# Kernel tuning notes

Hardware: AMD Instinct MI355X
Metric: run time of the kernel (lower is better)

## Reference

```python
import jax, jax.numpy as jnp
import numpy as np
from functools import partial

DN = ('NCHW', 'OIHW', 'NCHW')

def conv2d(x, w, b, stride):
    y = jax.lax.conv_general_dilated(x, w, (stride, stride), 'VALID', dimension_numbers=DN)
    return y + b[None, :, None, None]

def squash(s, eps=1e-8):
    norm = jnp.linalg.norm(s, axis=-1, keepdims=True)
    return (norm ** 2 / (1 + norm ** 2)) * s / (norm + eps)

def setup_inputs() -> dict:
    key = jax.random.key(0)
    ks = jax.random.split(key, 10)
    B, H, W = 16, 32, 512
    F, CAPS, E, OD = 64, 8, 8, 16
    H1 = (H - 6) // 2 + 1          # 14
    W1 = (W - 6) // 2 + 1          # 254
    N = F * H1 * W1 // CAPS        # 28448
    s = 0.05
    return {
        'x': jax.random.normal(ks[0], (B, H, W), jnp.float32),
        'conv1_w': jax.random.normal(ks[1], (F, 1, 6, 6), jnp.float32) * s,
        'conv1_b': jnp.zeros((F,), jnp.float32),
        'conv2_w': jax.random.normal(ks[2], (F, F, 6, 6), jnp.float32) * s,
        'conv2_b': jnp.zeros((F,), jnp.float32),
        'conv3_w': jax.random.normal(ks[3], (F, 2 * F, 1, 1), jnp.float32) * s,
        'conv3_b': jnp.zeros((F,), jnp.float32),
        'pc_w': jax.random.normal(ks[4], (N, CAPS, CAPS), jnp.float32) * s,  # [N, in, out]
        'pc_b': jnp.zeros((N, CAPS), jnp.float32),
        'ec_w': jax.random.normal(ks[5], (N, E, OD, CAPS), jnp.float32),
    }

def reference(x, conv1_w, conv1_b, conv2_w, conv2_b, conv3_w, conv3_b, pc_w, pc_b, ec_w):
    CAPS = pc_w.shape[1]
    NUM_ITER = 3
    B = x.shape[0]
    h = x[:, None]                                  # [B,1,H,W]
    h = jax.nn.relu(conv2d(h, conv1_w, conv1_b, 2)) # [B,F,14,254]
    y = jnp.pad(h, ((0, 0), (0, 0), (2, 3), (2, 3)))  # ZeroPad2d((2,3,2,3))
    y = jax.nn.relu(conv2d(y, conv2_w, conv2_b, 1))
    h = jax.nn.relu(jnp.concatenate((h, y), axis=1))
    h = conv2d(h, conv3_w, conv3_b, 1)              # [B,F,14,254]
    u_in = h.reshape(B, -1, CAPS)                   # [B,N,caps_len]
    # PrimaryCaps: N independent Linear(caps,caps) -> one batched einsum
    u = jnp.einsum('bni,nio->bno', u_in, pc_w) + pc_b[None]
    # EmotionCaps: per-capsule prediction u_hat [B,N,E,out_dim]
    u_hat = jnp.einsum('neoi,bni->bneo', ec_w, u)
    N, E = ec_w.shape[0], ec_w.shape[1]
    b_log = jnp.zeros((B, N, E), u_hat.dtype)
    v = None
    for r in range(NUM_ITER):
        c = jax.nn.softmax(b_log, axis=2)           # [B,N,E]
        s = jnp.einsum('bne,bneo->beo', c, u_hat)   # [B,E,out_dim]
        v = squash(s)
        if r < NUM_ITER - 1:
            b_log = b_log + jnp.einsum('bneo,beo->bne', u_hat, v)
    return jnp.linalg.norm(v, axis=-1)              # [B,E]
```

## Files before the change

### kernel.cpp

```cpp
#include <hip/hip_runtime.h>
#include <hip/hip_bf16.h>
#include <math.h>

#define BB 16
#define H1 14
#define W1 254
#define HPH 19
#define HPW2 264
#define NCAP 28448
#define FLATSZ 227584

typedef __attribute__((ext_vector_type(8))) short bf16x8;
typedef __attribute__((ext_vector_type(4))) float f32x4;
typedef __attribute__((ext_vector_type(2))) __fp16 f16x2;
typedef __attribute__((ext_vector_type(8))) _Float16 h8;
typedef __attribute__((ext_vector_type(4))) uint uint4v;

__device__ __forceinline__ ushort f2bf(float f) {
  __hip_bfloat16 h = __float2bfloat16(f);
  return *(ushort*)&h;
}

__global__ __launch_bounds__(256) void prep_w(const float* __restrict__ w2, const float* __restrict__ w3,
                                              ushort* __restrict__ wb, float* __restrict__ w3t) {
  int idx = blockIdx.x * 256 + threadIdx.x;
  if (idx < 147456) {
    int co = idx / 2304; int rem = idx - co * 2304;
    int tap = rem >> 6; int ci = rem & 63;
    wb[idx] = f2bf(w2[(co * 64 + ci) * 36 + tap]);
  }
  if (idx < 8192) {
    int co = idx & 63; int c = idx >> 6;
    w3t[idx] = w3[co * 128 + c];
  }
}

__global__ __launch_bounds__(256) void cvt_ec(const float* __restrict__ ecw, uint* __restrict__ ech) {
  size_t i = (size_t)blockIdx.x * 256 + threadIdx.x;
  const float4* s = (const float4*)ecw + i * 2;
  float4 a = s[0], b = s[1];
  uint4v pk;
  { f16x2 h = __builtin_amdgcn_cvt_pkrtz(a.x, a.y); pk.x = *(uint*)&h; }
  { f16x2 h = __builtin_amdgcn_cvt_pkrtz(a.z, a.w); pk.y = *(uint*)&h; }
  { f16x2 h = __builtin_amdgcn_cvt_pkrtz(b.x, b.y); pk.z = *(uint*)&h; }
  { f16x2 h = __builtin_amdgcn_cvt_pkrtz(b.z, b.w); pk.w = *(uint*)&h; }
  *((uint4v*)ech + i) = pk;
}

__global__ __launch_bounds__(256) void cvt_u(const float* __restrict__ u, _Float16* __restrict__ uh) {
  const int idx = blockIdx.x * 256 + threadIdx.x;
  const int n = idx >> 4, b = idx & 15;
  const float4* s = (const float4*)(u + ((size_t)b * NCAP + n) * 8);
  float4 xa = s[0], xb = s[1];
  h8 o;
  o[0] = (_Float16)xa.x; o[1] = (_Float16)xa.y; o[2] = (_Float16)xa.z; o[3] = (_Float16)xa.w;
  o[4] = (_Float16)xb.x; o[5] = (_Float16)xb.y; o[6] = (_Float16)xb.z; o[7] = (_Float16)xb.w;
  *(h8*)(uh + (size_t)idx * 8) = o;
}

__global__ __launch_bounds__(256) void conv1_k(const float* __restrict__ x, const float* __restrict__ w1,
                                               const float* __restrict__ b1, float* __restrict__ hc) {
  const int i = blockIdx.x, b = blockIdx.y;
  __shared__ float xs[6 * 512];
  __shared__ float wsh[2304];
  __shared__ float bsh[64];
  const int t = threadIdx.x;
  for (int idx = t; idx < 6 * 512; idx += 256) {
    int r = idx >> 9, c = idx & 511;
    xs[idx] = x[((size_t)b * 32 + 2 * i + r) * 512 + c];
  }
  for (int idx = t; idx < 2304; idx += 256) wsh[idx] = w1[idx];
  if (t < 64) bsh[t] = b1[t];
  __syncthreads();
  if (t < 254) {
    for (int c = 0; c < 64; c++) {
      float acc = bsh[c];
#pragma unroll
      for (int p = 0; p < 6; p++)
#pragma unroll
        for (int q = 0; q < 6; q++)
          acc = fmaf(xs[p * 512 + 2 * t + q], wsh[c * 36 + p * 6 + q], acc);
      acc = fmaxf(acc, 0.f);
      hc[(((size_t)b * 64 + c) * H1 + i) * W1 + t] = acc;
    }
  }
}

__global__ __launch_bounds__(256) void nhwc_k(const float* __restrict__ hc, ushort* __restrict__ hpc) {
  const int ct = blockIdx.x, i = blockIdx.y, b = blockIdx.z;
  const int c0 = ct * 64;
  __shared__ float ls[64 * 65];
  const int t = threadIdx.x;
  for (int idx = t; idx < 4096; idx += 256) {
    int ci = idx >> 6, cc = idx & 63;
    int c = c0 + cc;
    ls[ci * 65 + cc] = (c < W1) ? hc[(((size_t)b * 64 + ci) * H1 + i) * W1 + c] : 0.f;
  }
  __syncthreads();
  uint* outp = (uint*)hpc;
  for (int idx = t; idx < 2048; idx += 256) {
    int cc = idx >> 5, ci2 = idx & 31;
    int c = c0 + cc;
    if (c < W1) {
      float f0 = ls[(2 * ci2) * 65 + cc];
      float f1 = ls[(2 * ci2 + 1) * 65 + cc];
      uint pk = (uint)f2bf(f0) | ((uint)f2bf(f1) << 16);
      outp[(((size_t)b * HPH + 2 + i) * HPW2 + 2 + c) * 32 + ci2] = pk;
    }
  }
}

__device__ __forceinline__ void stage_b(const ushort* __restrict__ wb, ushort* __restrict__ bbuf,
                                        int tap, int w, int l) {
#pragma unroll
  for (int r = 0; r < 2; r++) {
    int v = r * 256 + w * 64 + l;
    int co = v >> 3, s = v & 7;
    int g = s ^ (co & 7);
    const ushort* gp = wb + co * 2304 + tap * 64 + g * 8;
    ushort* lp = bbuf + (size_t)(r * 256 + w * 64) * 8;
    __builtin_amdgcn_global_load_lds((const uint*)gp, (uint*)lp, 16, 0, 0);
  }
}

__global__ __launch_bounds__(256, 1) void conv2_mfma(const ushort* __restrict__ hpc,
                                                     const ushort* __restrict__ wb,
                                                     const float* __restrict__ b2, float* __restrict__ y) {
  const int b = blockIdx.z, i = blockIdx.y, j0 = blockIdx.x * 128;
  const int t = threadIdx.x;
  const int w = t >> 6, l = t & 63;
  const int lr = l & 15, quad = l >> 4;

  __shared__ ushort bls[2][4096];

  f32x4 acc[2][4];
#pragma unroll
  for (int mt = 0; mt < 2; mt++)
#pragma unroll
    for (int nt = 0; nt < 4; nt++) acc[mt][nt] = (f32x4){0.f, 0.f, 0.f, 0.f};

  const ushort* abase = hpc + (((size_t)b * HPH + i) * HPW2 + (j0 + w * 32 + lr)) * 64 + quad * 8;

  bf16x8 a0[2][2], a1[2][2];

#define ALOAD(dst, tap)                                                        \
  {                                                                            \
    const int p_ = (tap) / 6, q_ = (tap) % 6;                                  \
    const ushort* ap_ = abase + ((size_t)p_ * HPW2 + q_) * 64;                 \
    dst[0][0] = *(const bf16x8*)(ap_);                                         \
    dst[0][1] = *(const bf16x8*)(ap_ + 1024);                                  \
    dst[1][0] = *(const bf16x8*)(ap_ + 32);                                    \
    dst[1][1] = *(const bf16x8*)(ap_ + 32 + 1024);                             \
  }

#define COMPUTE(a, bp)                                                         \
  {                                                                            \
    _Pragma("unroll")                                                          \
    for (int ch = 0; ch < 2; ch++) {                                           \
      const int g2 = ch * 4 + quad;                                            \
      _Pragma("unroll")                                                        \
      for (int nt = 0; nt < 4; nt++) {                                         \
        const int co = nt * 16 + lr;                                           \
        bf16x8 bf = *(const bf16x8*)((bp) + co * 64 + ((g2 ^ (co & 7)) * 8));  \
        acc[0][nt] = __builtin_amdgcn_mfma_f32_16x16x32_bf16(a[ch][0], bf, acc[0][nt], 0, 0, 0); \
        acc[1][nt] = __builtin_amdgcn_mfma_f32_16x16x32_bf16(a[ch][1], bf, acc[1][nt], 0, 0, 0); \
      }                                                                        \
    }                                                                          \
  }

  stage_b(wb, &bls[0][0], 0, w, l);
  __syncthreads();
  ALOAD(a0, 0);

  for (int tp = 0; tp < 36; tp += 2) {
    stage_b(wb, &bls[1][0], tp + 1, w, l);
    ALOAD(a1, tp + 1);
    COMPUTE(a0, &bls[0][0]);
    __syncthreads();
    if (tp + 2 < 36) {
      stage_b(wb, &bls[0][0], tp + 2, w, l);
      ALOAD(a0, tp + 2);
    }
    COMPUTE(a1, &bls[1][0]);
    __syncthreads();
  }

#pragma unroll
  for (int nt = 0; nt < 4; nt++) {
    const int co = nt * 16 + lr;
    const float bias = b2[co];
    float* yrow = y + (((size_t)b * 64 + co) * H1 + i) * W1;
#pragma unroll
    for (int mt = 0; mt < 2; mt++) {
      const int jb = j0 + w * 32 + mt * 16 + quad * 4;
#pragma unroll
      for (int r = 0; r < 4; r++) {
        int j = jb + r;
        if (j < W1) yrow[j] = fmaxf(acc[mt][nt][r] + bias, 0.f);
      }
    }
  }
#undef ALOAD
#undef COMPUTE
}

__global__ __launch_bounds__(256) void conv3_k(const float* __restrict__ hc, const float* __restrict__ y,
                                               const float* __restrict__ w3t, const float* __restrict__ b3,
                                               float* __restrict__ out3) {
  const int b = blockIdx.z, i = blockIdx.y, j0 = blockIdx.x * 64;
  __shared__ float cs[32][64];
  __shared__ float wsh[32][64];
  const int t = threadIdx.x;
  const int cog = t >> 4, jg = t & 15;
  float acc[4][4];
#pragma unroll
  for (int a = 0; a < 4; a++)
#pragma unroll
    for (int j = 0; j < 4; j++) acc[a][j] = 0.f;

  for (int ch = 0; ch < 4; ch++) {
    __syncthreads();
    for (int idx = t; idx < 2048; idx += 256) {
      int cl = idx >> 6; int j = j0 + (idx & 63);
      int c = ch * 32 + cl;
      float v = 0.f;
      if (j < W1) {
        if (c < 64) v = hc[(((size_t)b * 64 + c) * H1 + i) * W1 + j];
        else        v = y[(((size_t)b * 64 + (c - 64)) * H1 + i) * W1 + j];
      }
      cs[cl][idx & 63] = v;
    }
    for (int idx = t; idx < 2048; idx += 256)
      wsh[idx >> 6][idx & 63] = w3t[(ch * 32 + (idx >> 6)) * 64 + (idx & 63)];
    __syncthreads();
#pragma unroll
    for (int c = 0; c < 32; c++) {
      float4 xv = *(const float4*)&cs[c][jg * 4];
      float4 wv = *(const float4*)&wsh[c][cog * 4];
#pragma unroll
      for (int jj = 0; jj < 4; jj++) {
        float xx = (&xv.x)[jj];
        acc[0][jj] = fmaf(wv.x, xx, acc[0][jj]);
        acc[1][jj] = fmaf(wv.y, xx, acc[1][jj]);
        acc[2][jj] = fmaf(wv.z, xx, acc[2][jj]);
        acc[3][jj] = fmaf(wv.w, xx, acc[3][jj]);
      }
    }
  }
#pragma unroll
  for (int a = 0; a < 4; a++) {
    int co = cog * 4 + a;
    float bias = b3[co];
#pragma unroll
    for (int jj = 0; jj < 4; jj++) {
      int j = j0 + jg * 4 + jj;
      if (j < W1) out3[(((size_t)b * 64 + co) * H1 + i) * W1 + j] = acc[a][jj] + bias;
    }
  }
}

__global__ __launch_bounds__(256) void pc_k(const float* __restrict__ out3, const float* __restrict__ pcw,
                                            const float* __restrict__ pcb, float* __restrict__ u) {
  int n = blockIdx.x * 256 + threadIdx.x;
  if (n >= NCAP) return;
  float pw[64];
  const float4* pwp = (const float4*)(pcw + (size_t)n * 64);
#pragma unroll
  for (int k = 0; k < 16; k++) {
    float4 v = pwp[k];
    pw[4 * k] = v.x; pw[4 * k + 1] = v.y; pw[4 * k + 2] = v.z; pw[4 * k + 3] = v.w;
  }
  float pb[8];
  {
    const float4* pbp = (const float4*)(pcb + (size_t)n * 8);
    float4 a = pbp[0], b = pbp[1];
    pb[0] = a.x; pb[1] = a.y; pb[2] = a.z; pb[3] = a.w;
    pb[4] = b.x; pb[5] = b.y; pb[6] = b.z; pb[7] = b.w;
  }
  for (int b = 0; b < BB; b++) {
    const float4* uip = (const float4*)(out3 + (size_t)b * FLATSZ + (size_t)n * 8);
    float4 a = uip[0], c = uip[1];
    float ui[8] = {a.x, a.y, a.z, a.w, c.x, c.y, c.z, c.w};
    float uo[8];
#pragma unroll
    for (int o = 0; o < 8; o++) uo[o] = pb[o];
#pragma unroll
    for (int i2 = 0; i2 < 8; i2++)
#pragma unroll
      for (int o = 0; o < 8; o++) uo[o] = fmaf(ui[i2], pw[i2 * 8 + o], uo[o]);
    float4* up = (float4*)(u + ((size_t)b * NCAP + n) * 8);
    up[0] = make_float4(uo[0], uo[1], uo[2], uo[3]);
    up[1] = make_float4(uo[4], uo[5], uo[6], uo[7]);
  }
}

template <int CTRL>
__device__ __forceinline__ float dpp_add(float x) {
  int y = __builtin_amdgcn_update_dpp(0, __float_as_int(x), CTRL, 0xF, 0xF, true);
  return x + __int_as_float(y);
}

__device__ __forceinline__ float xor32_partner(float x, bool low) {
#if __has_builtin(__builtin_amdgcn_permlane32_swap)
  auto r = __builtin_amdgcn_permlane32_swap(__float_as_uint(x), __float_as_uint(x), false, false);
  return __uint_as_float(low ? r[1] : r[0]);
#else
  return __uint_as_float((uint)__builtin_amdgcn_ds_bpermute(
      (int)((((threadIdx.x & 63) ^ 32) << 2)), (int)__float_as_uint(x)));
#endif
}

__global__ __launch_bounds__(256, 4) void route_s0(const _Float16* __restrict__ uh,
                                                   const _Float16* __restrict__ ech,
                                                   float* __restrict__ sout) {
  __shared__ float red[8192];
  const int t = threadIdx.x, l = t & 63, wv = t >> 6;
  const int q = l >> 4, lo = l & 15;
  const int n0 = blockIdx.x * 32 + wv * 8;

  f32x4 sacc[8];
#pragma unroll
  for (int e = 0; e < 8; e++) sacc[e] = (f32x4){0.f, 0.f, 0.f, 0.f};

#pragma unroll 1
  for (int g = 0; g < 2; g++) {
    const int nb = n0 + g * 4;
    h8 a = *(const h8*)(uh + ((size_t)(nb + q) * 16 + lo) * 8);
#pragma unroll
    for (int e = 0; e < 8; e++) {
      h8 b = *(const h8*)(ech + (((size_t)(nb + q) * 8 + e) * 16 + lo) * 8);
      sacc[e] = __builtin_amdgcn_mfma_f32_16x16x32_f16(a, b, sacc[e], 0, 0, 0);
    }
  }

#pragma unroll
  for (int e = 0; e < 8; e++)
#pragma unroll
    for (int r = 0; r < 4; r++)
      red[wv * 2048 + (4 * q + r) * 128 + e * 16 + lo] = sacc[e][r];
  __syncthreads();
#pragma unroll
  for (int m = 0; m < 8; m++) {
    const int slot = t + 256 * m;
    atomicAdd(&sout[slot], red[slot] + red[2048 + slot] + red[4096 + slot] + red[6144 + slot]);
  }
}

__global__ __launch_bounds__(256, 4) void route_s1(const float* __restrict__ u, const uint* __restrict__ ech,
                                                   const float* __restrict__ v, float* __restrict__ sout) {
  __shared__ float red[4096];
  float* us = red;

  const int t = threadIdx.x, l = t & 63, wv = t >> 6;
  const int b0 = blockIdx.y * 8;
  const int n0 = blockIdx.x * 32 + wv * 8;
  const bool low = l < 32;

  float2 vv[8];
#pragma unroll
  for (int bb = 0; bb < 8; bb++)
    vv[bb] = *(const float2*)&v[(size_t)(b0 + bb) * 128 + 2 * l];

#pragma unroll
  for (int bb = 0; bb < 8; bb++)
    us[wv * 512 + bb * 64 + l] = u[((size_t)(b0 + bb) * NCAP + n0) * 8 + l];

  float sacc[16];
#pragma unroll
  for (int k = 0; k < 16; k++) sacc[k] = 0.f;

  const uint4v* hbase = (const uint4v*)(ech + (size_t)n0 * 512) + (l * 2);

  auto proc = [&](int nn, uint4v w0, uint4v w1) {
    float ec[16];
#pragma unroll
    for (int k = 0; k < 4; k++) {
      uint t0 = w0[k], t1 = w1[k];
      f16x2 a = *(f16x2*)&t0;
      f16x2 b = *(f16x2*)&t1;
      ec[2 * k]     = (float)a.x; ec[2 * k + 1] = (float)a.y;
      ec[8 + 2 * k] = (float)b.x; ec[8 + 2 * k + 1] = (float)b.y;
    }
#pragma unroll
    for (int bb = 0; bb < 8; bb++) {
      const float4* up = (const float4*)&us[wv * 512 + bb * 64 + nn * 8];
      const float4 ua = up[0], ub = up[1];
      const float uv[8] = {ua.x, ua.y, ua.z, ua.w, ub.x, ub.y, ub.z, ub.w};
      float h0 = 0.f, h1 = 0.f;
#pragma unroll
      for (int k = 0; k < 8; k++) {
        h0 = fmaf(ec[k], uv[k], h0);
        h1 = fmaf(ec[8 + k], uv[k], h1);
      }
      float p = fmaf(h0, vv[bb].x, h1 * vv[bb].y);
      p = dpp_add<0xB1>(p);
      p = dpp_add<0x4E>(p);
      p = dpp_add<0x141>(p);
      const float ex = __expf(p);
      float den = dpp_add<0x140>(ex);
      den += __int_as_float(__builtin_amdgcn_ds_swizzle(__float_as_int(den), 0x401F));
      den += xor32_partner(den, low);
      const float cc = ex * __builtin_amdgcn_rcpf(den);
      sacc[2 * bb] = fmaf(cc, h0, sacc[2 * bb]);
      sacc[2 * bb + 1] = fmaf(cc, h1, sacc[2 * bb + 1]);
    }
  };

  uint4v ca0 = hbase[0], ca1 = hbase[1];
#pragma unroll 1
  for (int nn = 0; nn < 8; nn += 2) {
    const uint4v* pb = hbase + (size_t)(nn + 1) * 128;
    uint4v cb0 = pb[0], cb1 = pb[1];
    proc(nn, ca0, ca1);
    if (nn + 2 < 8) {
      const uint4v* pa = hbase + (size_t)(nn + 2) * 128;
      ca0 = pa[0]; ca1 = pa[1];
    }
    proc(nn + 1, cb0, cb1);
  }

  __syncthreads();
#pragma unroll
  for (int k = 0; k < 16; k++) red[k * 256 + wv * 64 + l] = sacc[k];
  __syncthreads();
#pragma unroll
  for (int m = 0; m < 4; m++) {
    int slot = t + 256 * m;
    int bl = slot >> 7, eo = slot & 127;
    int k = 2 * bl + (eo & 1), l2 = eo >> 1;
    const float* r = red + k * 256 + l2;
    atomicAdd(&sout[(b0 + bl) * 128 + eo], r[0] + r[64] + r[128] + r[192]);
  }
}

__global__ void squash_k(const float* __restrict__ s, float scale, const float* __restrict__ vprev,
                         float* __restrict__ vout) {
  int t = threadIdx.x;
  const float* sp = s + t * 16;
  float sv[16]; float nn = 0.f;
#pragma unroll
  for (int o = 0; o < 16; o++) { float x = sp[o] * scale; sv[o] = x; nn = fmaf(x, x, nn); }
  float norm = sqrtf(nn);
  float f = nn / (1.f + nn) / (norm + 1e-8f);
#pragma unroll
  for (int o = 0; o < 16; o++) {
    float base = vprev ? vprev[t * 16 + o] : 0.f;
    vout[t * 16 + o] = base + f * sv[o];
  }
}

__global__ void squash_out_k(const float* __restrict__ s, float* __restrict__ out) {
  int t = threadIdx.x;
  float nn = 0.f;
#pragma unroll
  for (int o = 0; o < 16; o++) { float x = s[t * 16 + o]; nn = fmaf(x, x, nn); }
  float norm = sqrtf(nn);
  float f = nn / (1.f + nn) / (norm + 1e-8f);
  out[t] = f * norm;
}

extern "C" void kernel_launch(void* const* d_in, const int* in_sizes, int n_in,
                              void* d_out, int out_size, void* d_ws, size_t ws_size,
                              hipStream_t stream) {
  const float* x   = (const float*)d_in[0];
  const float* w1  = (const float*)d_in[1];
  const float* b1  = (const float*)d_in[2];
  const float* w2  = (const float*)d_in[3];
  const float* b2  = (const float*)d_in[4];
  const float* w3  = (const float*)d_in[5];
  const float* b3  = (const float*)d_in[6];
  const float* pcw = (const float*)d_in[7];
  const float* pcb = (const float*)d_in[8];
  const float* ecw = (const float*)d_in[9];
  float* out = (float*)d_out;

  float* ws = (float*)d_ws;
  size_t o = 0;
  float* hc   = ws + o; o += 3641344;
  float* yb   = ws + o; o += 3641344;
  float* out3 = ws + o; o += 3641344;
  ushort* hpc = (ushort*)(ws + o); o += 2568192;
  ushort* wb  = (ushort*)(ws + o); o += 73728;
  float* w3t  = ws + o; o += 8192;
  float* s0   = ws + o; o += 2048;
  float* s1   = ws + o; o += 2048;
  float* s2   = ws + o; o += 2048;
  float* v0   = ws + o; o += 2048;
  float* v1   = ws + o; o += 2048;
  uint* ech   = (uint*)(ws + o); o += 14565376;
  float* ub   = hc;
  _Float16* uhp = (_Float16*)yb;

  hipMemsetAsync(hpc, 0, (size_t)16 * HPH * HPW2 * 64 * 2, stream);
  hipMemsetAsync(s0, 0, 3 * 2048 * 4, stream);

  prep_w<<<576, 256, 0, stream>>>(w2, w3, wb, w3t);
  cvt_ec<<<14224, 256, 0, stream>>>(ecw, ech);
  conv1_k<<<dim3(14, 16), 256, 0, stream>>>(x, w1, b1, hc);
  nhwc_k<<<dim3(4, 14, 16), 256, 0, stream>>>(hc, hpc);
  conv2_mfma<<<dim3(2, 14, 16), 256, 0, stream>>>(hpc, wb, b2, yb);
  conv3_k<<<dim3(4, 14, 16), 256, 0, stream>>>(hc, yb, w3t, b3, out3);
  pc_k<<<112, 256, 0, stream>>>(out3, pcw, pcb, ub);
  cvt_u<<<1778, 256, 0, stream>>>(ub, uhp);

  route_s0<<<889, 256, 0, stream>>>(uhp, (const _Float16*)ech, s0);
  squash_k<<<1, 128, 0, stream>>>(s0, 0.125f, nullptr, v0);
  route_s1<<<dim3(889, 2), 256, 0, stream>>>(ub, ech, v0, s1);
  squash_k<<<1, 128, 0, stream>>>(s1, 1.0f, v0, v1);
  route_s1<<<dim3(889, 2), 256, 0, stream>>>(ub, ech, v1, s2);
  squash_out_k<<<1, 128, 0, stream>>>(s2, out);
}
```

Measured before the change: 472.6 us.

## Fuse ec weight conversion into first routing pass and squash into route kernels

Removes the separate cvt_ec kernel and does the fp32-to-fp16 conversion of ec_w inside the first routing kernel, which writes the packed copy for later passes while using it directly in the MFMA. The single-block squash kernels are dropped; each route_s1 pass recomputes v from the raw s sums with DPP reductions. pc_k gets a second grid dimension over batch halves to add parallelism. The aim is fewer launches and one fewer full pass over the large ec_w tensor. In exchange the squash math is recomputed redundantly per block.

```diff
diff --git a/kernel.cpp b/kernel.cpp
--- a/kernel.cpp
+++ b/kernel.cpp
@@ -33,18 +33,6 @@
     int co = idx & 63; int c = idx >> 6;
     w3t[idx] = w3[co * 128 + c];
   }
-}
-
-__global__ __launch_bounds__(256) void cvt_ec(const float* __restrict__ ecw, uint* __restrict__ ech) {
-  size_t i = (size_t)blockIdx.x * 256 + threadIdx.x;
-  const float4* s = (const float4*)ecw + i * 2;
-  float4 a = s[0], b = s[1];
-  uint4v pk;
-  { f16x2 h = __builtin_amdgcn_cvt_pkrtz(a.x, a.y); pk.x = *(uint*)&h; }
-  { f16x2 h = __builtin_amdgcn_cvt_pkrtz(a.z, a.w); pk.y = *(uint*)&h; }
-  { f16x2 h = __builtin_amdgcn_cvt_pkrtz(b.x, b.y); pk.z = *(uint*)&h; }
-  { f16x2 h = __builtin_amdgcn_cvt_pkrtz(b.z, b.w); pk.w = *(uint*)&h; }
-  *((uint4v*)ech + i) = pk;
 }
 
 __global__ __launch_bounds__(256) void cvt_u(const float* __restrict__ u, _Float16* __restrict__ uh) {
@@ -263,6 +251,7 @@
                                             const float* __restrict__ pcb, float* __restrict__ u) {
   int n = blockIdx.x * 256 + threadIdx.x;
   if (n >= NCAP) return;
+  const int bb0 = blockIdx.y * 8;
   float pw[64];
   const float4* pwp = (const float4*)(pcw + (size_t)n * 64);
 #pragma unroll
@@ -277,7 +266,7 @@
     pb[0] = a.x; pb[1] = a.y; pb[2] = a.z; pb[3] = a.w;
     pb[4] = b.x; pb[5] = b.y; pb[6] = b.z; pb[7] = b.w;
   }
-  for (int b = 0; b < BB; b++) {
+  for (int b = bb0; b < bb0 + 8; b++) {
     const float4* uip = (const float4*)(out3 + (size_t)b * FLATSZ + (size_t)n * 8);
     float4 a = uip[0], c = uip[1];
     float ui[8] = {a.x, a.y, a.z, a.w, c.x, c.y, c.z, c.w};
@@ -310,9 +299,10 @@
 #endif
 }
 
-__global__ __launch_bounds__(256, 4) void route_s0(const _Float16* __restrict__ uh,
-                                                   const _Float16* __restrict__ ech,
-                                                   float* __restrict__ sout) {
+__global__ __launch_bounds__(256, 4) void route_cvt0(const _Float16* __restrict__ uh,
+                                                     const float* __restrict__ ecw,
+                                                     uint4v* __restrict__ ech4,
+                                                     float* __restrict__ sout) {
   __shared__ float red[8192];
   const int t = threadIdx.x, l = t & 63, wv = t >> 6;
   const int q = l >> 4, lo = l & 15;
@@ -324,12 +314,21 @@
 
 #pragma unroll 1
   for (int g = 0; g < 2; g++) {
-    const int nb = n0 + g * 4;
-    h8 a = *(const h8*)(uh + ((size_t)(nb + q) * 16 + lo) * 8);
+    const int n = n0 + g * 4 + q;
+    h8 a = *(const h8*)(uh + ((size_t)n * 16 + lo) * 8);
 #pragma unroll
     for (int e = 0; e < 8; e++) {
-      h8 b = *(const h8*)(ech + (((size_t)(nb + q) * 8 + e) * 16 + lo) * 8);
-      sacc[e] = __builtin_amdgcn_mfma_f32_16x16x32_f16(a, b, sacc[e], 0, 0, 0);
+      const size_t eoff = ((size_t)n * 8 + e) * 16 + lo;
+      const float4* wp = (const float4*)(ecw + eoff * 8);
+      const float4 w0 = wp[0], w1 = wp[1];
+      uint4v pk;
+      { f16x2 h = __builtin_amdgcn_cvt_pkrtz(w0.x, w0.y); pk.x = *(uint*)&h; }
+      { f16x2 h = __builtin_amdgcn_cvt_pkrtz(w0.z, w0.w); pk.y = *(uint*)&h; }
+      { f16x2 h = __builtin_amdgcn_cvt_pkrtz(w1.x, w1.y); pk.z = *(uint*)&h; }
+      { f16x2 h = __builtin_amdgcn_cvt_pkrtz(w1.z, w1.w); pk.w = *(uint*)&h; }
+      ech4[eoff] = pk;
+      h8 bv = *(h8*)&pk;
+      sacc[e] = __builtin_amdgcn_mfma_f32_16x16x32_f16(a, bv, sacc[e], 0, 0, 0);
     }
   }
 
@@ -346,8 +345,10 @@
   }
 }
 
+template <int PASS>
 __global__ __launch_bounds__(256, 4) void route_s1(const float* __restrict__ u, const uint* __restrict__ ech,
-                                                   const float* __restrict__ v, float* __restrict__ sout) {
+                                                   const float* __restrict__ s0g, const float* __restrict__ s1g,
+                                                   float* __restrict__ sout) {
   __shared__ float red[4096];
   float* us = red;
 
@@ -358,8 +359,21 @@
 
   float2 vv[8];
 #pragma unroll
-  for (int bb = 0; bb < 8; bb++)
-    vv[bb] = *(const float2*)&v[(size_t)(b0 + bb) * 128 + 2 * l];
+  for (int bb = 0; bb < 8; bb++) {
+    float2 sp = *(const float2*)&s0g[(size_t)(b0 + bb) * 128 + 2 * l];
+    sp.x *= 0.125f; sp.y *= 0.125f;
+    float q2 = fmaf(sp.x, sp.x, sp.y * sp.y);
+    q2 = dpp_add<0xB1>(q2); q2 = dpp_add<0x4E>(q2); q2 = dpp_add<0x141>(q2);
+    float f = q2 / (1.f + q2) / (sqrtf(q2) + 1e-8f);
+    vv[bb].x = f * sp.x; vv[bb].y = f * sp.y;
+    if (PASS == 2) {
+      float2 sq = *(const float2*)&s1g[(size_t)(b0 + bb) * 128 + 2 * l];
+      float r2 = fmaf(sq.x, sq.x, sq.y * sq.y);
+      r2 = dpp_add<0xB1>(r2); r2 = dpp_add<0x4E>(r2); r2 = dpp_add<0x141>(r2);
+      float g2 = r2 / (1.f + r2) / (sqrtf(r2) + 1e-8f);
+      vv[bb].x = fmaf(g2, sq.x, vv[bb].x); vv[bb].y = fmaf(g2, sq.y, vv[bb].y);
+    }
+  }
 
 #pragma unroll
   for (int bb = 0; bb < 8; bb++)
@@ -430,22 +444,6 @@
     int k = 2 * bl + (eo & 1), l2 = eo >> 1;
     const float* r = red + k * 256 + l2;
     atomicAdd(&sout[(b0 + bl) * 128 + eo], r[0] + r[64] + r[128] + r[192]);
-  }
-}
-
-__global__ void squash_k(const float* __restrict__ s, float scale, const float* __restrict__ vprev,
-                         float* __restrict__ vout) {
-  int t = threadIdx.x;
-  const float* sp = s + t * 16;
-  float sv[16]; float nn = 0.f;
-#pragma unroll
-  for (int o = 0; o < 16; o++) { float x = sp[o] * scale; sv[o] = x; nn = fmaf(x, x, nn); }
-  float norm = sqrtf(nn);
-  float f = nn / (1.f + nn) / (norm + 1e-8f);
-#pragma unroll
-  for (int o = 0; o < 16; o++) {
-    float base = vprev ? vprev[t * 16 + o] : 0.f;
-    vout[t * 16 + o] = base + f * sv[o];
   }
 }
 
@@ -490,23 +488,21 @@
   uint* ech   = (uint*)(ws + o); o += 14565376;
   float* ub   = hc;
   _Float16* uhp = (_Float16*)yb;
+  (void)v0; (void)v1;
 
   hipMemsetAsync(hpc, 0, (size_t)16 * HPH * HPW2 * 64 * 2, stream);
   hipMemsetAsync(s0, 0, 3 * 2048 * 4, stream);
 
   prep_w<<<576, 256, 0, stream>>>(w2, w3, wb, w3t);
-  cvt_ec<<<14224, 256, 0, stream>>>(ecw, ech);
   conv1_k<<<dim3(14, 16), 256, 0, stream>>>(x, w1, b1, hc);
   nhwc_k<<<dim3(4, 14, 16), 256, 0, stream>>>(hc, hpc);
   conv2_mfma<<<dim3(2, 14, 16), 256, 0, stream>>>(hpc, wb, b2, yb);
   conv3_k<<<dim3(4, 14, 16), 256, 0, stream>>>(hc, yb, w3t, b3, out3);
-  pc_k<<<112, 256, 0, stream>>>(out3, pcw, pcb, ub);
+  pc_k<<<dim3(112, 2), 256, 0, stream>>>(out3, pcw, pcb, ub);
   cvt_u<<<1778, 256, 0, stream>>>(ub, uhp);
 
-  route_s0<<<889, 256, 0, stream>>>(uhp, (const _Float16*)ech, s0);
-  squash_k<<<1, 128, 0, stream>>>(s0, 0.125f, nullptr, v0);
-  route_s1<<<dim3(889, 2), 256, 0, stream>>>(ub, ech, v0, s1);
-  squash_k<<<1, 128, 0, stream>>>(s1, 1.0f, v0, v1);
-  route_s1<<<dim3(889, 2), 256, 0, stream>>>(ub, ech, v1, s2);
+  route_cvt0<<<889, 256, 0, stream>>>(uhp, ecw, (uint4v*)ech, s0);
+  route_s1<1><<<dim3(889, 2), 256, 0, stream>>>(ub, ech, s0, nullptr, s1);
+  route_s1<2><<<dim3(889, 2), 256, 0, stream>>>(ub, ech, s0, s1, s2);
   squash_out_k<<<1, 128, 0, stream>>>(s2, out);
 }
```

Result: faster. 443.4 us (-6.2%).
